# Optimization experiments

Measured on AMD Instinct MI355X. Metric: run time of the kernel, lower is better.

Reference implementation:

```python
import jax, jax.numpy as jnp
import numpy as np

T, H, F, E, K, C = 8192, 1024, 2048, 16, 2, 1280  # tokens, hidden, ffn, experts, top_k, capacity


def setup_inputs() -> dict:
    key = jax.random.key(0)
    ks = jax.random.split(key, 6)
    return {
        "x": jax.random.normal(ks[0], (T, H), dtype=jnp.float32),
        "w_router": jax.random.normal(ks[1], (H, E), dtype=jnp.float32) * 0.02,
        "w1": jax.random.normal(ks[2], (E, H, F), dtype=jnp.float32) * 0.02,
        "b1": jnp.zeros((E, F), dtype=jnp.float32),
        "w2": jax.random.normal(ks[3], (E, F, H), dtype=jnp.float32) * 0.02,
        "b2": jnp.zeros((E, H), dtype=jnp.float32),
    }


def reference(x, w_router, w1, b1, w2, b2):
    # ---- Router: softmax + top-k (TopKRouter) ----
    logits = x @ w_router                                  # [T, E]
    probs = jax.nn.softmax(logits, axis=-1)
    topk_p, topk_idx = jax.lax.top_k(probs, K)             # [T, K]
    topk_p = topk_p / jnp.sum(topk_p, axis=-1, keepdims=True)

    # ---- Dispatch with capacity drop (token_permutation) ----
    flat_e = topk_idx.reshape(-1)                          # [T*K] expert id per assignment
    token_ids = jnp.repeat(jnp.arange(T), K)               # [T*K]
    oh = jax.nn.one_hot(flat_e, E, dtype=jnp.int32)        # [T*K, E]
    # position of each assignment within its expert's buffer (token order)
    pos = jnp.cumsum(oh, axis=0) - oh                      # [T*K, E]
    pos = jnp.take_along_axis(pos, flat_e[:, None], axis=1)[:, 0]  # [T*K]
    keep = pos < C
    safe_pos = jnp.where(keep, pos, C)                     # dropped tokens -> dummy slot C

    dispatched = jnp.zeros((E, C + 1, H), dtype=x.dtype)
    dispatched = dispatched.at[flat_e, safe_pos].add(x[token_ids])
    disp = dispatched[:, :C, :]                            # [E, C, H]

    # ---- Grouped expert MLP (SequentialMLP: fc1 -> gelu -> fc2) ----
    h = jax.nn.gelu(jnp.einsum("ech,ehf->ecf", disp, w1) + b1[:, None, :])
    y = jnp.einsum("ecf,efh->ech", h, w2) + b2[:, None, :]  # [E, C, H]

    # ---- Combine (token_unpermutation): gather + prob-weighted sum ----
    y_pad = jnp.pad(y, ((0, 0), (0, 1), (0, 0)))            # dummy slot returns garbage, masked below
    gathered = y_pad[flat_e, safe_pos]                      # [T*K, H]
    gathered = jnp.where(keep[:, None], gathered, 0.0)
    weighted = gathered * topk_p.reshape(-1)[:, None]
    out = jax.ops.segment_sum(weighted, token_ids, num_segments=T)  # [T, H]
    return out
```

## Files before the change

kernel.cpp:

```cpp
#include <hip/hip_runtime.h>
#include <cstdint>
#include <cstddef>

#define T_TOK 8192
#define HDIM  1024
#define FDIM  2048
#define NEXP  16
#define CAP   1280

typedef __bf16 bf16x8 __attribute__((ext_vector_type(8)));
typedef float  f32x4  __attribute__((ext_vector_type(4)));

__device__ inline void gld16(const void* g, void* l) {
  __builtin_amdgcn_global_load_lds(
      (__attribute__((address_space(1))) void*)g,
      (__attribute__((address_space(3))) void*)l, 16, 0, 0);
}

__global__ __launch_bounds__(256) void router_kernel(
    const float* __restrict__ x, const float* __restrict__ wr,
    int* __restrict__ eidx, float* __restrict__ eprob) {
  int t = blockIdx.x * 4 + (threadIdx.x >> 6);
  int lane = threadIdx.x & 63;
  float acc[NEXP];
#pragma unroll
  for (int e = 0; e < NEXP; ++e) acc[e] = 0.f;
  const float4* xp = (const float4*)(x + (size_t)t * HDIM + lane * 16);
#pragma unroll
  for (int q = 0; q < 4; ++q) {
    float4 xv = xp[q];
    float xa[4] = {xv.x, xv.y, xv.z, xv.w};
#pragma unroll
    for (int ii = 0; ii < 4; ++ii) {
      int h = lane * 16 + q * 4 + ii;
      const float4* wp = (const float4*)(wr + (size_t)h * NEXP);
      float w[NEXP];
      float4 w0 = wp[0], w1 = wp[1], w2 = wp[2], w3 = wp[3];
      w[0]=w0.x; w[1]=w0.y; w[2]=w0.z; w[3]=w0.w;
      w[4]=w1.x; w[5]=w1.y; w[6]=w1.z; w[7]=w1.w;
      w[8]=w2.x; w[9]=w2.y; w[10]=w2.z; w[11]=w2.w;
      w[12]=w3.x; w[13]=w3.y; w[14]=w3.z; w[15]=w3.w;
#pragma unroll
      for (int e = 0; e < NEXP; ++e) acc[e] += xa[ii] * w[e];
    }
  }
#pragma unroll
  for (int e = 0; e < NEXP; ++e) {
#pragma unroll
    for (int s = 32; s > 0; s >>= 1) acc[e] += __shfl_xor(acc[e], s);
  }
  if (lane == 0) {
    float l0 = -1e30f, l1 = -1e30f; int i0 = 0, i1 = 0;
#pragma unroll
    for (int e = 0; e < NEXP; ++e) {
      float v = acc[e];
      if (v > l0) { l1 = l0; i1 = i0; l0 = v; i0 = e; }
      else if (v > l1) { l1 = v; i1 = e; }
    }
    float p0 = 1.f / (1.f + __expf(l1 - l0));
    eidx[t * 2 + 0] = i0; eidx[t * 2 + 1] = i1;
    eprob[t * 2 + 0] = p0; eprob[t * 2 + 1] = 1.f - p0;
  }
}

__global__ __launch_bounds__(256) void pos_kernel(
    const int* __restrict__ eidx, const float* __restrict__ eprob,
    int* __restrict__ slot_token, float* __restrict__ slot_prob) {
  __shared__ int scan[256][NEXP];
  int tid = threadIdx.x;
  int cnt[NEXP];
#pragma unroll
  for (int e = 0; e < NEXP; ++e) cnt[e] = 0;
  int base_i = tid * 64;
  const int4* ep = (const int4*)(eidx + base_i);
  for (int i = 0; i < 16; ++i) {
    int4 v = ep[i];
    cnt[v.x]++; cnt[v.y]++; cnt[v.z]++; cnt[v.w]++;
  }
#pragma unroll
  for (int e = 0; e < NEXP; ++e) scan[tid][e] = cnt[e];
  __syncthreads();
  if (tid < NEXP) {
    int run = 0;
    for (int i = 0; i < 256; ++i) { int v = scan[i][tid]; scan[i][tid] = run; run += v; }
  }
  __syncthreads();
  int basec[NEXP];
#pragma unroll
  for (int e = 0; e < NEXP; ++e) basec[e] = scan[tid][e];
  for (int i = 0; i < 64; ++i) {
    int fi = base_i + i;
    int e = eidx[fi];
    int p = basec[e]++;
    if (p < CAP) {
      slot_token[e * CAP + p] = fi >> 1;
      slot_prob[e * CAP + p] = eprob[fi];
    }
  }
}

__global__ __launch_bounds__(256) void scatter_kernel(
    const float* __restrict__ x, const int* __restrict__ slot_token,
    __bf16* __restrict__ disp) {
  int s = blockIdx.x * 4 + (threadIdx.x >> 6);
  int lane = threadIdx.x & 63;
  int tok = slot_token[s];
  __bf16 vals[16] __attribute__((aligned(16)));
  if (tok >= 0) {
    const float4* xp = (const float4*)(x + (size_t)tok * HDIM + lane * 16);
#pragma unroll
    for (int q = 0; q < 4; ++q) {
      float4 v = xp[q];
      vals[q * 4 + 0] = (__bf16)v.x; vals[q * 4 + 1] = (__bf16)v.y;
      vals[q * 4 + 2] = (__bf16)v.z; vals[q * 4 + 3] = (__bf16)v.w;
    }
  } else {
#pragma unroll
    for (int q = 0; q < 16; ++q) vals[q] = (__bf16)0.f;
  }
  uint4* dst = (uint4*)(disp + (size_t)s * HDIM + lane * 16);
  dst[0] = ((uint4*)vals)[0];
  dst[1] = ((uint4*)vals)[1];
}

__global__ __launch_bounds__(256) void transpose_cast_kernel(
    const float* __restrict__ src, __bf16* __restrict__ dst, int R, int Cc) {
  int e = blockIdx.z;
  src += (size_t)e * R * Cc;
  dst += (size_t)e * R * Cc;
  __shared__ float tile[64][65];
  int gy = blockIdx.y * 64;
  int gx = blockIdx.x * 64;
  int tid = threadIdx.x;
  int r = tid >> 4;
  int c4 = (tid & 15) * 4;
#pragma unroll
  for (int rr = 0; rr < 4; ++rr) {
    float4 v = *(const float4*)(src + (size_t)(gy + r + rr * 16) * Cc + gx + c4);
    tile[r + rr * 16][c4 + 0] = v.x;
    tile[r + rr * 16][c4 + 1] = v.y;
    tile[r + rr * 16][c4 + 2] = v.z;
    tile[r + rr * 16][c4 + 3] = v.w;
  }
  __syncthreads();
  int r2 = tid >> 2;
  int cb = (tid & 3) * 16;
  __bf16 o[16] __attribute__((aligned(16)));
#pragma unroll
  for (int i = 0; i < 16; ++i) o[i] = (__bf16)tile[cb + i][r2];
  uint4* dp = (uint4*)(dst + (size_t)(gx + r2) * R + gy + cb);
  dp[0] = ((uint4*)o)[0];
  dp[1] = ((uint4*)o)[1];
}

template <int EPI, int KSPLIT>
__global__ __launch_bounds__(512, 2) void moe_gemm_kernel(
    const __bf16* __restrict__ A, const __bf16* __restrict__ Bt,
    const float* __restrict__ bias, __bf16* __restrict__ Hout,
    const int* __restrict__ slot_token, const float* __restrict__ slot_prob,
    float* __restrict__ out, int M, int N, int Kd) {
  const int e  = blockIdx.z / KSPLIT;
  const int ks = blockIdx.z % KSPLIT;
  const int m0 = blockIdx.y * 256, n0 = blockIdx.x * 256;
  const __bf16* Ae = A + (size_t)e * M * Kd;
  const __bf16* Be = Bt + (size_t)e * N * Kd;
  __shared__ __bf16 lds[4 * 16384];
  const int tid = threadIdx.x, wave = tid >> 6, lane = tid & 63;
  const int quad = lane >> 4, l15 = lane & 15;
  const int wm = (wave >> 2) * 128, wn = (wave & 3) * 64;
  f32x4 acc[8][4] = {};
  const int Kb = Kd * 2;
  const int ktiles = (Kd / KSPLIT) >> 5;
  const int kbase = ks * (Kd / KSPLIT) * 2;

  const int bofs0 = wave * 2048;
  int srow[2], sgcol[2];
#pragma unroll
  for (int rr = 0; rr < 2; ++rr) {
    int lofs = bofs0 + rr * 1024 + lane * 16;
    int row = lofs >> 6;
    int chunk = (lofs >> 4) & 3;
    srow[rr] = row;
    sgcol[rr] = (chunk ^ ((row >> 1) & 3)) * 16;
  }

  auto stage = [&](int kt) {
    char* dstA = (char*)lds + (kt & 3) * 32768;
    char* dstB = dstA + 16384;
#pragma unroll
    for (int rr = 0; rr < 2; ++rr) {
      int bofs = bofs0 + rr * 1024;
      gld16((const char*)Ae + (size_t)(m0 + srow[rr]) * Kb + kbase + kt * 64 + sgcol[rr],
            dstA + bofs);
      gld16((const char*)Be + (size_t)(n0 + srow[rr]) * Kb + kbase + kt * 64 + sgcol[rr],
            dstB + bofs);
    }
  };

  stage(0);
  if (ktiles > 1) stage(1);
  if (ktiles > 2) stage(2);
  for (int kt = 0; kt < ktiles; ++kt) {
    int rem = ktiles - kt;
    if (rem >= 3)      __builtin_amdgcn_s_waitcnt(0x0f78);
    else if (rem == 2) __builtin_amdgcn_s_waitcnt(0x0f74);
    else               __builtin_amdgcn_s_waitcnt(0x0f70);
    __builtin_amdgcn_s_barrier();
    if (kt + 3 < ktiles) stage(kt + 3);
    const __bf16* La = lds + (kt & 3) * 16384;
    const __bf16* Lb = La + 8192;
    bf16x8 av[8], bv[4];
#pragma unroll
    for (int i = 0; i < 8; ++i) {
      int r = wm + i * 16 + l15;
      av[i] = *(const bf16x8*)&La[r * 32 + ((quad ^ ((r >> 1) & 3)) << 3)];
    }
#pragma unroll
    for (int j = 0; j < 4; ++j) {
      int r = wn + j * 16 + l15;
      bv[j] = *(const bf16x8*)&Lb[r * 32 + ((quad ^ ((r >> 1) & 3)) << 3)];
    }
#pragma unroll
    for (int i = 0; i < 8; ++i)
#pragma unroll
      for (int j = 0; j < 4; ++j)
        acc[i][j] = __builtin_amdgcn_mfma_f32_16x16x32_bf16(av[i], bv[j], acc[i][j], 0, 0, 0);
  }
  if (EPI == 1) {
    __bf16* He = Hout + (size_t)e * M * N;
    float bj[4];
#pragma unroll
    for (int j = 0; j < 4; ++j) bj[j] = bias[(size_t)e * N + n0 + wn + j * 16 + l15];
#pragma unroll
    for (int i = 0; i < 8; ++i) {
#pragma unroll
      for (int r = 0; r < 4; ++r) {
        int m = m0 + wm + i * 16 + quad * 4 + r;
#pragma unroll
        for (int j = 0; j < 4; ++j) {
          int n = n0 + wn + j * 16 + l15;
          float v = acc[i][j][r] + bj[j];
          float u = 0.7978845608028654f * (v + 0.044715f * v * v * v);
          float ex = __expf(-2.f * fabsf(u));
          float th = (1.f - ex) / (1.f + ex);
          th = copysignf(th, u);
          He[(size_t)m * N + n] = (__bf16)(0.5f * v * (1.f + th));
        }
      }
    }
  } else {
    const int* st = slot_token + e * CAP;
    const float* sp = slot_prob + e * CAP;
    float bj[4];
#pragma unroll
    for (int j = 0; j < 4; ++j)
      bj[j] = (ks == 0) ? bias[(size_t)e * N + n0 + wn + j * 16 + l15] : 0.f;
#pragma unroll
    for (int i = 0; i < 8; ++i) {
#pragma unroll
      for (int r = 0; r < 4; ++r) {
        int m = m0 + wm + i * 16 + quad * 4 + r;
        int tok = st[m];
        if (tok >= 0) {
          float p = sp[m];
#pragma unroll
          for (int j = 0; j < 4; ++j) {
            int n = n0 + wn + j * 16 + l15;
            float v = acc[i][j][r] + bj[j];
            atomicAdd(out + (size_t)tok * HDIM + n, p * v);
          }
        }
      }
    }
  }
}

extern "C" void kernel_launch(void* const* d_in, const int* in_sizes, int n_in,
                              void* d_out, int out_size, void* d_ws, size_t ws_size,
                              hipStream_t stream) {
  const float* x  = (const float*)d_in[0];
  const float* wr = (const float*)d_in[1];
  const float* w1 = (const float*)d_in[2];
  const float* b1 = (const float*)d_in[3];
  const float* w2 = (const float*)d_in[4];
  const float* b2 = (const float*)d_in[5];
  float* out = (float*)d_out;

  char* ws = (char*)d_ws;
  size_t off = 0;
  __bf16* w1t = (__bf16*)(ws + off); off += (size_t)NEXP * FDIM * HDIM * 2;
  __bf16* w2t = (__bf16*)(ws + off); off += (size_t)NEXP * HDIM * FDIM * 2;
  __bf16* disp = (__bf16*)(ws + off); off += (size_t)NEXP * CAP * HDIM * 2;
  __bf16* hbuf = (__bf16*)(ws + off); off += (size_t)NEXP * CAP * FDIM * 2;
  int*   slot_token = (int*)(ws + off);  off += (size_t)NEXP * CAP * 4;
  float* slot_prob  = (float*)(ws + off); off += (size_t)NEXP * CAP * 4;
  int*   eidx  = (int*)(ws + off);  off += (size_t)T_TOK * 2 * 4;
  float* eprob = (float*)(ws + off); off += (size_t)T_TOK * 2 * 4;
  if (ws_size < off) return;

  hipMemsetAsync(slot_token, 0xFF, (size_t)NEXP * CAP * 4, stream);
  hipMemsetAsync(d_out, 0, (size_t)T_TOK * HDIM * 4, stream);

  transpose_cast_kernel<<<dim3(FDIM / 64, HDIM / 64, NEXP), 256, 0, stream>>>(w1, w1t, HDIM, FDIM);
  transpose_cast_kernel<<<dim3(HDIM / 64, FDIM / 64, NEXP), 256, 0, stream>>>(w2, w2t, FDIM, HDIM);

  router_kernel<<<T_TOK / 4, 256, 0, stream>>>(x, wr, eidx, eprob);
  pos_kernel<<<1, 256, 0, stream>>>(eidx, eprob, slot_token, slot_prob);
  scatter_kernel<<<NEXP * CAP / 4, 256, 0, stream>>>(x, slot_token, disp);

  moe_gemm_kernel<1, 1><<<dim3(FDIM / 256, CAP / 256, NEXP), 512, 0, stream>>>(
      disp, w1t, b1, hbuf, nullptr, nullptr, nullptr, CAP, FDIM, HDIM);
  moe_gemm_kernel<2, 2><<<dim3(HDIM / 256, CAP / 256, NEXP * 2), 512, 0, stream>>>(
      hbuf, w2t, b2, nullptr, slot_token, slot_prob, out, CAP, HDIM, FDIM);
}
```

Before: 798.1 us.

## Restructure MoE GEMM main loop to double-buffered K=64 tiles with XOR swizzle

Replaces the 4-stage K=32 LDS ring with a 2-stage double buffer holding K=64 tiles (128 bytes per row). The XOR swizzle is now 8-way over 16-byte chunks, and the A/B LDS offsets are precomputed. The loop has one barrier per 64-wide K step, and s_setprio is raised around the MFMA block. The goal is fewer barriers and waitcnt stalls per unit of work and fewer LDS bank conflicts, at the cost of shallower prefetch depth, which may expose more global load latency. LDS use stays at 128 KB, which may limit occupancy under launch_bounds(512,2).

```diff
diff --git a/kernel.cpp b/kernel.cpp
--- a/kernel.cpp
+++ b/kernel.cpp
@@ -162,69 +162,66 @@
   const int e  = blockIdx.z / KSPLIT;
   const int ks = blockIdx.z % KSPLIT;
   const int m0 = blockIdx.y * 256, n0 = blockIdx.x * 256;
-  const __bf16* Ae = A + (size_t)e * M * Kd;
-  const __bf16* Be = Bt + (size_t)e * N * Kd;
-  __shared__ __bf16 lds[4 * 16384];
+  const char* Ae = (const char*)A + (size_t)e * M * Kd * 2;
+  const char* Be = (const char*)Bt + (size_t)e * N * Kd * 2;
+  __shared__ __bf16 lds[2 * 32768];
   const int tid = threadIdx.x, wave = tid >> 6, lane = tid & 63;
   const int quad = lane >> 4, l15 = lane & 15;
   const int wm = (wave >> 2) * 128, wn = (wave & 3) * 64;
   f32x4 acc[8][4] = {};
-  const int Kb = Kd * 2;
-  const int ktiles = (Kd / KSPLIT) >> 5;
+  const size_t Kb = (size_t)Kd * 2;
+  const int ktiles = (Kd / KSPLIT) >> 6;
   const int kbase = ks * (Kd / KSPLIT) * 2;
 
-  const int bofs0 = wave * 2048;
-  int srow[2], sgcol[2];
-#pragma unroll
-  for (int rr = 0; rr < 2; ++rr) {
-    int lofs = bofs0 + rr * 1024 + lane * 16;
-    int row = lofs >> 6;
-    int chunk = (lofs >> 4) & 3;
-    srow[rr] = row;
-    sgcol[rr] = (chunk ^ ((row >> 1) & 3)) * 16;
-  }
-
-  auto stage = [&](int kt) {
-    char* dstA = (char*)lds + (kt & 3) * 32768;
-    char* dstB = dstA + 16384;
-#pragma unroll
-    for (int rr = 0; rr < 2; ++rr) {
-      int bofs = bofs0 + rr * 1024;
-      gld16((const char*)Ae + (size_t)(m0 + srow[rr]) * Kb + kbase + kt * 64 + sgcol[rr],
-            dstA + bofs);
-      gld16((const char*)Be + (size_t)(n0 + srow[rr]) * Kb + kbase + kt * 64 + sgcol[rr],
-            dstB + bofs);
-    }
+  const int rbase = tid >> 3;
+  const int scol  = ((tid & 7) ^ ((tid >> 3) & 7)) * 16;
+  const char* srcA = Ae + (size_t)(m0 + rbase) * Kb + kbase + scol;
+  const char* srcB = Be + (size_t)(n0 + rbase) * Kb + kbase + scol;
+  const size_t rstep = 64 * Kb;
+  const int dofs = tid * 16;
+
+  auto stage = [&](int t) {
+    char* base = (char*)lds + (t & 1) * 65536;
+#pragma unroll
+    for (int j = 0; j < 4; ++j)
+      gld16(srcA + (size_t)t * 128 + j * rstep, base + dofs + j * 8192);
+#pragma unroll
+    for (int j = 0; j < 4; ++j)
+      gld16(srcB + (size_t)t * 128 + j * rstep, base + 32768 + dofs + j * 8192);
   };
 
+  int aoff[8], boff[4], coff[2];
+#pragma unroll
+  for (int i = 0; i < 8; ++i) aoff[i] = (wm + i * 16 + l15) * 128;
+#pragma unroll
+  for (int j = 0; j < 4; ++j) boff[j] = (wn + j * 16 + l15) * 128;
+#pragma unroll
+  for (int kk = 0; kk < 2; ++kk) coff[kk] = (((kk * 4 + quad) ^ (l15 & 7)) * 16);
+
   stage(0);
-  if (ktiles > 1) stage(1);
-  if (ktiles > 2) stage(2);
-  for (int kt = 0; kt < ktiles; ++kt) {
-    int rem = ktiles - kt;
-    if (rem >= 3)      __builtin_amdgcn_s_waitcnt(0x0f78);
-    else if (rem == 2) __builtin_amdgcn_s_waitcnt(0x0f74);
-    else               __builtin_amdgcn_s_waitcnt(0x0f70);
+  __builtin_amdgcn_s_waitcnt(0x0f70);
+  __builtin_amdgcn_s_barrier();
+  for (int t = 0; t < ktiles; ++t) {
+    if (t + 1 < ktiles) stage(t + 1);
+    const char* La = (const char*)lds + (t & 1) * 65536;
+    const char* Lb = La + 32768;
+#pragma unroll
+    for (int kk = 0; kk < 2; ++kk) {
+      bf16x8 av[8], bv[4];
+#pragma unroll
+      for (int i = 0; i < 8; ++i) av[i] = *(const bf16x8*)(La + aoff[i] + coff[kk]);
+#pragma unroll
+      for (int j = 0; j < 4; ++j) bv[j] = *(const bf16x8*)(Lb + boff[j] + coff[kk]);
+      __builtin_amdgcn_s_setprio(1);
+#pragma unroll
+      for (int i = 0; i < 8; ++i)
+#pragma unroll
+        for (int j = 0; j < 4; ++j)
+          acc[i][j] = __builtin_amdgcn_mfma_f32_16x16x32_bf16(av[i], bv[j], acc[i][j], 0, 0, 0);
+      __builtin_amdgcn_s_setprio(0);
+    }
+    if (t + 1 < ktiles) __builtin_amdgcn_s_waitcnt(0x0f70);
     __builtin_amdgcn_s_barrier();
-    if (kt + 3 < ktiles) stage(kt + 3);
-    const __bf16* La = lds + (kt & 3) * 16384;
-    const __bf16* Lb = La + 8192;
-    bf16x8 av[8], bv[4];
-#pragma unroll
-    for (int i = 0; i < 8; ++i) {
-      int r = wm + i * 16 + l15;
-      av[i] = *(const bf16x8*)&La[r * 32 + ((quad ^ ((r >> 1) & 3)) << 3)];
-    }
-#pragma unroll
-    for (int j = 0; j < 4; ++j) {
-      int r = wn + j * 16 + l15;
-      bv[j] = *(const bf16x8*)&Lb[r * 32 + ((quad ^ ((r >> 1) & 3)) << 3)];
-    }
-#pragma unroll
-    for (int i = 0; i < 8; ++i)
-#pragma unroll
-      for (int j = 0; j < 4; ++j)
-        acc[i][j] = __builtin_amdgcn_mfma_f32_16x16x32_bf16(av[i], bv[j], acc[i][j], 0, 0, 0);
   }
   if (EPI == 1) {
     __bf16* He = Hout + (size_t)e * M * N;
```

Result: faster. 780.2 us (-2.2%).
